# Kernel tuning notes

Measured on AMD Instinct MI355X. Metric: run time of the kernel, lower is better.

The kernel has to match this reference:

```python
import jax, jax.numpy as jnp
import numpy as np

EPS = 1e-5  # F.normalize eps


def _l2norm(x):
    # torch F.normalize(p=2): x / max(||x||, eps)
    n = jnp.sqrt(jnp.sum(x * x, axis=-1, keepdims=True))
    return x / jnp.maximum(n, EPS)


def setup_inputs() -> dict:
    B, L, D, T = 32, 128, 256, 10000
    key = jax.random.key(0)
    ks = jax.random.split(key, 10)
    data = jax.random.normal(ks[0], (B, L, D), jnp.float32)
    # event ids in [1, T]; 0 is the padding id (none here, so packing matches original loop)
    event_type = jax.random.randint(ks[1], (B, L), 1, T + 1, dtype=jnp.int32)
    emb_table = jax.random.normal(ks[2], (T + 1, D), jnp.float32)
    place_correlation = jax.random.uniform(ks[3], (T, T), jnp.float32)
    xav = np.sqrt(2.0 / (T + D))  # xavier_normal_ std for Linear(dim, num_types)
    W5 = jax.random.normal(ks[4], (T, D), jnp.float32) * xav
    W1 = jax.random.normal(ks[5], (T, D), jnp.float32) * xav
    W2 = jax.random.normal(ks[6], (T, D), jnp.float32) * xav
    W3 = jax.random.normal(ks[7], (T, D), jnp.float32) * xav
    W4 = jax.random.normal(ks[8], (T, D), jnp.float32) * xav
    one = jnp.ones((1,), jnp.float32)
    # F.dropout(p=0.5, training=True): precomputed keep-mask already scaled by 1/(1-p)=2
    drop_mask = jax.random.bernoulli(ks[9], 0.5, (B, L, T)).astype(jnp.float32) * 2.0
    return dict(data=data, event_type=event_type, emb_table=emb_table,
                place_correlation=place_correlation, W1=W1, W2=W2, W3=W3, W4=W4,
                W5=W5, a=one, b=one, c=one, d=one, drop_mask=drop_mask)


def reference(data, event_type, emb_table, place_correlation,
              W1, W2, W3, W4, W5, a, b, c, d, drop_mask):
    B = data.shape[0]
    T = W5.shape[0]
    # event_emb(event_type).detach()
    event_enc = jax.lax.stop_gradient(emb_table[event_type])           # [B,L,D]
    inner = jnp.tanh(jnp.einsum('bld,td->blt', event_enc, W5)) * drop_mask  # [B,L,T]
    valid = event_type != 0                                            # pad mask
    idx = jnp.where(valid, event_type - 1, 0)                          # [B,L]
    # per-event gather of correlation rows, fused multiply + reduce over L
    corr = place_correlation[idx] * valid[..., None].astype(place_correlation.dtype)  # [B,L,T]
    item = _l2norm(jnp.sum(inner * corr, axis=1))                      # [B,T]
    # target_: ones, zeroed at observed event indices
    rows = jnp.arange(B)[:, None]
    target = jnp.ones((B, T), jnp.float32).at[rows, idx].min(
        jnp.where(valid, 0.0, 1.0).astype(jnp.float32))
    dm = jnp.mean(data, axis=1)                                        # [B,D]
    p = lambda W: _l2norm(dm @ W.T)
    out = jnp.tanh(p(W1) * a + p(W2) * b + p(W3) * c + p(W4) * d + item)
    return out, target
```

## Files before the change

### kernel.cpp

```cpp
#include <hip/hip_runtime.h>
#include <hip/hip_bf16.h>
#include <stdint.h>

#define T_DIM 10000
#define B_DIM 32
#define L_DIM 128
#define D_DIM 256
#define NT_TILES 79
#define TPAD (NT_TILES*128)

typedef __bf16 bf16x8 __attribute__((ext_vector_type(8)));
typedef float  f32x4  __attribute__((ext_vector_type(4)));
typedef unsigned short us8 __attribute__((ext_vector_type(8)));
typedef unsigned short ushort_t;

__device__ __forceinline__ unsigned short f2bf(float f){
  union { float f; uint32_t u; } v; v.f = f;
  uint32_t u = v.u;
  return (unsigned short)((u + 0x7fffu + ((u >> 16) & 1u)) >> 16);
}

__device__ __forceinline__ void async16(const void* g, void* l){
  __builtin_amdgcn_global_load_lds((const __attribute__((address_space(1))) void*)g,
                                   (__attribute__((address_space(3))) void*)l,
                                   16, 0, 0);
}

__device__ __forceinline__ float fast_tanh(float x){
  x = fminf(8.f, fmaxf(-8.f, x));
  float e = __expf(2.f * x);
  return (e - 1.f) * __builtin_amdgcn_rcpf(e + 1.f);
}

__global__ __launch_bounds__(256) void k_prep(
    const float* __restrict__ emb, const int* __restrict__ et,
    const float* __restrict__ W5, const float* __restrict__ data,
    ushort_t* __restrict__ ebf, ushort_t* __restrict__ w5b,
    ushort_t* __restrict__ dmb, float* __restrict__ tgt){
  int bx = blockIdx.x, tid = threadIdx.x;
  if (bx < 1024){
    int r = bx * 4 + (tid >> 6), d4 = tid & 63;
    int e = et[r];
    float4 v = *((const float4*)(emb + (size_t)e * D_DIM) + d4);
    ushort4 o; o.x = f2bf(v.x); o.y = f2bf(v.y); o.z = f2bf(v.z); o.w = f2bf(v.w);
    *((ushort4*)(ebf + (size_t)r * D_DIM) + d4) = o;
  } else if (bx < 3552){
    int r = (bx - 1024) * 4 + (tid >> 6), d4 = tid & 63;
    ushort4 o = {0,0,0,0};
    if (r < T_DIM){
      float4 v = *((const float4*)(W5 + (size_t)r * D_DIM) + d4);
      o.x = f2bf(v.x); o.y = f2bf(v.y); o.z = f2bf(v.z); o.w = f2bf(v.w);
    }
    *((ushort4*)(w5b + (size_t)r * D_DIM) + d4) = o;
  } else if (bx < 3584){
    int b = bx - 3552, d = tid;
    const float* p = data + (size_t)b * L_DIM * D_DIM + d;
    float s = 0.f;
    #pragma unroll 4
    for (int l = 0; l < L_DIM; l++) s += p[(size_t)l * D_DIM];
    dmb[b * D_DIM + d] = f2bf(s * (1.0f / L_DIM));
  } else {
    int i = (bx - 3584) * 256 + tid;
    if (i < B_DIM * T_DIM) tgt[i] = 1.0f;
  }
}

__global__ __launch_bounds__(256, 4) void k_big(
    const ushort_t* __restrict__ ebf, const ushort_t* __restrict__ w5b,
    const float* __restrict__ corr, const float* __restrict__ drop,
    const int* __restrict__ et, float* __restrict__ item){
  __shared__ __align__(16) ushort_t lA[128 * 64];
  __shared__ __align__(16) ushort_t lB[128 * 64];
  const int b  = blockIdx.y;
  const int t0 = blockIdx.x * 128;
  const int tid = threadIdx.x;
  const int w = tid >> 6, lane = tid & 63, col = lane & 15, quad = lane >> 4;
  const int srow8 = lane >> 3, sslot = lane & 7;

  f32x4 zero4 = {0.f, 0.f, 0.f, 0.f};
  f32x4 acc[2][8];
  #pragma unroll
  for (int m = 0; m < 2; m++)
    #pragma unroll
    for (int n = 0; n < 8; n++) acc[m][n] = zero4;

  for (int c = 0; c < 4; c++){
    if (c) __syncthreads();
    #pragma unroll
    for (int it = 0; it < 4; it++){
      int rb = (it * 4 + w) * 8;
      int row = rb + srow8;
      int gseg = sslot ^ (row & 7);
      async16(ebf + (size_t)(b * L_DIM + row) * D_DIM + c * 64 + gseg * 8,
              lA + rb * 64);
      async16(w5b + (size_t)(t0 + row) * D_DIM + c * 64 + gseg * 8,
              lB + rb * 64);
    }
    __syncthreads();
    #pragma unroll
    for (int kk = 0; kk < 2; kk++){
      bf16x8 af[2];
      #pragma unroll
      for (int m = 0; m < 2; m++){
        int row = w * 32 + m * 16 + col;
        int sg = (kk * 4 + quad) ^ (row & 7);
        af[m] = *(const bf16x8*)(lA + row * 64 + sg * 8);
      }
      #pragma unroll
      for (int n = 0; n < 8; n++){
        int row = n * 16 + col;
        int sg = (kk * 4 + quad) ^ (row & 7);
        bf16x8 bf = *(const bf16x8*)(lB + row * 64 + sg * 8);
        acc[0][n] = __builtin_amdgcn_mfma_f32_16x16x32_bf16(af[0], bf, acc[0][n], 0, 0, 0);
        acc[1][n] = __builtin_amdgcn_mfma_f32_16x16x32_bf16(af[1], bf, acc[1][n], 0, 0, 0);
      }
    }
  }
  __syncthreads();

  int doff[8]; int coff[8]; float vm[8];
  #pragma unroll
  for (int m = 0; m < 2; m++)
    #pragma unroll
    for (int j = 0; j < 4; j++){
      int i = m * 4 + j;
      int l = w * 32 + m * 16 + quad * 4 + j;
      int e = et[b * L_DIM + l];
      doff[i] = (b * L_DIM + l) * T_DIM;
      coff[i] = (e > 0 ? e - 1 : 0) * T_DIM;
      vm[i] = (e > 0) ? 1.f : 0.f;
    }

  float* red = (float*)lA;
  #pragma unroll
  for (int n = 0; n < 8; n++){
    int t = t0 + n * 16 + col;
    bool tv = t < T_DIM;
    float s = 0.f;
    #pragma unroll
    for (int m = 0; m < 2; m++)
      #pragma unroll
      for (int j = 0; j < 4; j++){
        int i = m * 4 + j;
        float th = fast_tanh(acc[m][n][j]);
        float dv = tv ? drop[(size_t)doff[i] + t] : 0.f;
        float cv = tv ? corr[(size_t)coff[i] + t] : 0.f;
        s += th * dv * (cv * vm[i]);
      }
    s += __shfl_xor(s, 16);
    s += __shfl_xor(s, 32);
    if (lane < 16) red[w * 128 + n * 16 + col] = s;
  }
  __syncthreads();
  if (tid < 128){
    int t = t0 + tid;
    if (t < T_DIM)
      item[(size_t)b * T_DIM + t] = red[tid] + red[128 + tid] + red[256 + tid] + red[384 + tid];
  }
}

__global__ __launch_bounds__(256) void k_qgemm(
    const float* __restrict__ W1, const float* __restrict__ W2,
    const float* __restrict__ W3, const float* __restrict__ W4,
    const ushort_t* __restrict__ dmb, float* __restrict__ q){
  __shared__ __align__(16) ushort_t lB[128 * 128];
  const int kw = blockIdx.y;
  const float* W = (kw == 0) ? W1 : (kw == 1) ? W2 : (kw == 2) ? W3 : W4;
  const int t0 = blockIdx.x * 128;
  const int tid = threadIdx.x;
  const int w = tid >> 6, lane = tid & 63, col = lane & 15, quad = lane >> 4;

  f32x4 zero4 = {0.f, 0.f, 0.f, 0.f};
  f32x4 acc[2][2];
  acc[0][0] = zero4; acc[0][1] = zero4; acc[1][0] = zero4; acc[1][1] = zero4;

  for (int c = 0; c < 2; c++){
    if (c) __syncthreads();
    #pragma unroll
    for (int it = 0; it < 8; it++){
      int idx = it * 256 + tid;
      int row = idx >> 4, slot = idx & 15;
      int gseg = slot ^ (row & 7);
      int t = t0 + row;
      float4 u0 = {0,0,0,0}, u1 = {0,0,0,0};
      if (t < T_DIM){
        const float* gp = W + (size_t)t * D_DIM + c * 128 + gseg * 8;
        u0 = *(const float4*)gp;
        u1 = *(const float4*)(gp + 4);
      }
      us8 o;
      o[0] = f2bf(u0.x); o[1] = f2bf(u0.y); o[2] = f2bf(u0.z); o[3] = f2bf(u0.w);
      o[4] = f2bf(u1.x); o[5] = f2bf(u1.y); o[6] = f2bf(u1.z); o[7] = f2bf(u1.w);
      *(us8*)(lB + row * 128 + slot * 8) = o;
    }
    __syncthreads();
    #pragma unroll
    for (int kk = 0; kk < 4; kk++){
      int kabs = c * 128 + kk * 32 + quad * 8;
      bf16x8 af[2];
      #pragma unroll
      for (int m = 0; m < 2; m++)
        af[m] = *(const bf16x8*)(dmb + (size_t)(m * 16 + col) * D_DIM + kabs);
      #pragma unroll
      for (int n2 = 0; n2 < 2; n2++){
        int row = (w * 2 + n2) * 16 + col;
        int sg = (kk * 4 + quad) ^ (row & 7);
        bf16x8 bf = *(const bf16x8*)(lB + row * 128 + sg * 8);
        acc[0][n2] = __builtin_amdgcn_mfma_f32_16x16x32_bf16(af[0], bf, acc[0][n2], 0, 0, 0);
        acc[1][n2] = __builtin_amdgcn_mfma_f32_16x16x32_bf16(af[1], bf, acc[1][n2], 0, 0, 0);
      }
    }
  }
  #pragma unroll
  for (int m = 0; m < 2; m++)
    #pragma unroll
    for (int n2 = 0; n2 < 2; n2++)
      #pragma unroll
      for (int j = 0; j < 4; j++){
        int brow = m * 16 + quad * 4 + j;
        int t = t0 + (w * 2 + n2) * 16 + col;
        if (t < T_DIM)
          q[((size_t)kw * B_DIM + brow) * T_DIM + t] = acc[m][n2][j];
      }
}

__global__ __launch_bounds__(256) void k_norms(const float* __restrict__ q,
    const float* __restrict__ item, float* __restrict__ norms,
    const int* __restrict__ et, float* __restrict__ tgt){
  int which = blockIdx.x, b = blockIdx.y;
  if (which == 5){
    if (threadIdx.x < L_DIM){
      int e = et[b * L_DIM + threadIdx.x];
      if (e > 0) tgt[(size_t)b * T_DIM + (e - 1)] = 0.f;
    }
    return;
  }
  const float* src = (which < 4) ? (q + ((size_t)which * B_DIM + b) * T_DIM)
                                 : (item + (size_t)b * T_DIM);
  float s = 0.f;
  for (int i = threadIdx.x; i < T_DIM; i += 256){ float v = src[i]; s = fmaf(v, v, s); }
  #pragma unroll
  for (int o = 1; o < 64; o <<= 1) s += __shfl_xor(s, o);
  __shared__ float tmp[4];
  if ((threadIdx.x & 63) == 0) tmp[threadIdx.x >> 6] = s;
  __syncthreads();
  if (threadIdx.x == 0) norms[which * B_DIM + b] = sqrtf(tmp[0] + tmp[1] + tmp[2] + tmp[3]);
}

__global__ __launch_bounds__(256) void k_final(
    const float* __restrict__ q, const float* __restrict__ item,
    const float* __restrict__ norms,
    const float* __restrict__ pa, const float* __restrict__ pb,
    const float* __restrict__ pc, const float* __restrict__ pd,
    float* __restrict__ out){
  int b = blockIdx.y;
  int t = blockIdx.x * 256 + threadIdx.x;
  if (t >= T_DIM) return;
  float coef0 = *pa, coef1 = *pb, coef2 = *pc, coef3 = *pd;
  float v = item[(size_t)b * T_DIM + t] / fmaxf(norms[4 * B_DIM + b], 1e-5f);
  v += q[((size_t)0 * B_DIM + b) * T_DIM + t] * coef0 / fmaxf(norms[0 * B_DIM + b], 1e-5f);
  v += q[((size_t)1 * B_DIM + b) * T_DIM + t] * coef1 / fmaxf(norms[1 * B_DIM + b], 1e-5f);
  v += q[((size_t)2 * B_DIM + b) * T_DIM + t] * coef2 / fmaxf(norms[2 * B_DIM + b], 1e-5f);
  v += q[((size_t)3 * B_DIM + b) * T_DIM + t] * coef3 / fmaxf(norms[3 * B_DIM + b], 1e-5f);
  out[(size_t)b * T_DIM + t] = tanhf(v);
}

extern "C" void kernel_launch(void* const* d_in, const int* in_sizes, int n_in,
                              void* d_out, int out_size, void* d_ws, size_t ws_size,
                              hipStream_t stream){
  const float* data = (const float*)d_in[0];
  const int*   et   = (const int*)d_in[1];
  const float* emb  = (const float*)d_in[2];
  const float* corr = (const float*)d_in[3];
  const float* W1   = (const float*)d_in[4];
  const float* W2   = (const float*)d_in[5];
  const float* W3   = (const float*)d_in[6];
  const float* W4   = (const float*)d_in[7];
  const float* W5   = (const float*)d_in[8];
  const float* ca   = (const float*)d_in[9];
  const float* cb   = (const float*)d_in[10];
  const float* cc   = (const float*)d_in[11];
  const float* cd   = (const float*)d_in[12];
  const float* drop = (const float*)d_in[13];

  char* p = (char*)d_ws;
  ushort_t* ebf  = (ushort_t*)p; p += (size_t)B_DIM * L_DIM * D_DIM * 2;
  ushort_t* w5b  = (ushort_t*)p; p += (size_t)TPAD * D_DIM * 2;
  ushort_t* dmb  = (ushort_t*)p; p += (size_t)B_DIM * D_DIM * 2;
  float*    q    = (float*)p;    p += (size_t)4 * B_DIM * T_DIM * 4;
  float*    item = (float*)p;    p += (size_t)B_DIM * T_DIM * 4;
  float*    norms= (float*)p;    p += (size_t)5 * B_DIM * 4;

  float* out = (float*)d_out;
  float* tgt = out + (size_t)B_DIM * T_DIM;

  hipLaunchKernelGGL(k_prep,  dim3(4834),            dim3(256), 0, stream,
                     emb, et, W5, data, ebf, w5b, dmb, tgt);
  hipLaunchKernelGGL(k_big,   dim3(NT_TILES, B_DIM), dim3(256), 0, stream,
                     ebf, w5b, corr, drop, et, item);
  hipLaunchKernelGGL(k_qgemm, dim3(NT_TILES, 4),     dim3(256), 0, stream,
                     W1, W2, W3, W4, dmb, q);
  hipLaunchKernelGGL(k_norms, dim3(6, B_DIM),        dim3(256), 0, stream,
                     q, item, norms, et, tgt);
  hipLaunchKernelGGL(k_final, dim3(40, B_DIM),       dim3(256), 0, stream,
                     q, item, norms, ca, cb, cc, cd, out);
}
```

Baseline: 693.1 us.

## Fuse q-GEMM into main kernel and compute norms via atomic accumulation

Merges the W1-W4 projection GEMM into the main tanh/dropout/correlation kernel as extra block rows of one grid. Squared-norm partial sums are now accumulated with atomics in each GEMM epilogue, which removes the separate norms kernel and its re-read of q and item. The target scatter moves into the final kernel. This cuts two launches and one memory pass, but adds atomic traffic and summation order that is no longer deterministic.

```diff
diff --git a/kernel.cpp b/kernel.cpp
--- a/kernel.cpp
+++ b/kernel.cpp
@@ -36,7 +36,8 @@
     const float* __restrict__ emb, const int* __restrict__ et,
     const float* __restrict__ W5, const float* __restrict__ data,
     ushort_t* __restrict__ ebf, ushort_t* __restrict__ w5b,
-    ushort_t* __restrict__ dmb, float* __restrict__ tgt){
+    ushort_t* __restrict__ dmb, float* __restrict__ tgt,
+    float* __restrict__ norms2){
   int bx = blockIdx.x, tid = threadIdx.x;
   if (bx < 1024){
     int r = bx * 4 + (tid >> 6), d4 = tid & 63;
@@ -59,209 +60,211 @@
     #pragma unroll 4
     for (int l = 0; l < L_DIM; l++) s += p[(size_t)l * D_DIM];
     dmb[b * D_DIM + d] = f2bf(s * (1.0f / L_DIM));
-  } else {
+  } else if (bx < 4834){
     int i = (bx - 3584) * 256 + tid;
     if (i < B_DIM * T_DIM) tgt[i] = 1.0f;
+  } else {
+    if (tid < 160) norms2[tid] = 0.f;
   }
 }
 
-__global__ __launch_bounds__(256, 4) void k_big(
+__global__ __launch_bounds__(256, 4) void k_main(
     const ushort_t* __restrict__ ebf, const ushort_t* __restrict__ w5b,
     const float* __restrict__ corr, const float* __restrict__ drop,
-    const int* __restrict__ et, float* __restrict__ item){
-  __shared__ __align__(16) ushort_t lA[128 * 64];
-  __shared__ __align__(16) ushort_t lB[128 * 64];
-  const int b  = blockIdx.y;
+    const int* __restrict__ et, float* __restrict__ item,
+    const float* __restrict__ W1, const float* __restrict__ W2,
+    const float* __restrict__ W3, const float* __restrict__ W4,
+    const ushort_t* __restrict__ dmb, float* __restrict__ q,
+    float* __restrict__ norms2){
+  __shared__ __align__(16) ushort_t smem[128 * 128];
+  __shared__ float ssq[32];
   const int t0 = blockIdx.x * 128;
   const int tid = threadIdx.x;
   const int w = tid >> 6, lane = tid & 63, col = lane & 15, quad = lane >> 4;
-  const int srow8 = lane >> 3, sslot = lane & 7;
-
-  f32x4 zero4 = {0.f, 0.f, 0.f, 0.f};
-  f32x4 acc[2][8];
-  #pragma unroll
-  for (int m = 0; m < 2; m++)
-    #pragma unroll
-    for (int n = 0; n < 8; n++) acc[m][n] = zero4;
-
-  for (int c = 0; c < 4; c++){
-    if (c) __syncthreads();
-    #pragma unroll
-    for (int it = 0; it < 4; it++){
-      int rb = (it * 4 + w) * 8;
-      int row = rb + srow8;
-      int gseg = sslot ^ (row & 7);
-      async16(ebf + (size_t)(b * L_DIM + row) * D_DIM + c * 64 + gseg * 8,
-              lA + rb * 64);
-      async16(w5b + (size_t)(t0 + row) * D_DIM + c * 64 + gseg * 8,
-              lB + rb * 64);
+
+  if (blockIdx.y < B_DIM){
+    ushort_t* lA = smem;
+    ushort_t* lB = smem + 128 * 64;
+    const int b = blockIdx.y;
+    const int srow8 = lane >> 3, sslot = lane & 7;
+
+    f32x4 zero4 = {0.f, 0.f, 0.f, 0.f};
+    f32x4 acc[2][8];
+    #pragma unroll
+    for (int m = 0; m < 2; m++)
+      #pragma unroll
+      for (int n = 0; n < 8; n++) acc[m][n] = zero4;
+
+    for (int c = 0; c < 4; c++){
+      if (c) __syncthreads();
+      #pragma unroll
+      for (int it = 0; it < 4; it++){
+        int rb = (it * 4 + w) * 8;
+        int row = rb + srow8;
+        int gseg = sslot ^ (row & 7);
+        async16(ebf + (size_t)(b * L_DIM + row) * D_DIM + c * 64 + gseg * 8,
+                lA + rb * 64);
+        async16(w5b + (size_t)(t0 + row) * D_DIM + c * 64 + gseg * 8,
+                lB + rb * 64);
+      }
+      __syncthreads();
+      #pragma unroll
+      for (int kk = 0; kk < 2; kk++){
+        bf16x8 af[2];
+        #pragma unroll
+        for (int m = 0; m < 2; m++){
+          int row = w * 32 + m * 16 + col;
+          int sg = (kk * 4 + quad) ^ (row & 7);
+          af[m] = *(const bf16x8*)(lA + row * 64 + sg * 8);
+        }
+        #pragma unroll
+        for (int n = 0; n < 8; n++){
+          int row = n * 16 + col;
+          int sg = (kk * 4 + quad) ^ (row & 7);
+          bf16x8 bf = *(const bf16x8*)(lB + row * 64 + sg * 8);
+          acc[0][n] = __builtin_amdgcn_mfma_f32_16x16x32_bf16(af[0], bf, acc[0][n], 0, 0, 0);
+          acc[1][n] = __builtin_amdgcn_mfma_f32_16x16x32_bf16(af[1], bf, acc[1][n], 0, 0, 0);
+        }
+      }
     }
     __syncthreads();
-    #pragma unroll
-    for (int kk = 0; kk < 2; kk++){
-      bf16x8 af[2];
-      #pragma unroll
-      for (int m = 0; m < 2; m++){
-        int row = w * 32 + m * 16 + col;
-        int sg = (kk * 4 + quad) ^ (row & 7);
-        af[m] = *(const bf16x8*)(lA + row * 64 + sg * 8);
-      }
-      #pragma unroll
-      for (int n = 0; n < 8; n++){
-        int row = n * 16 + col;
-        int sg = (kk * 4 + quad) ^ (row & 7);
-        bf16x8 bf = *(const bf16x8*)(lB + row * 64 + sg * 8);
-        acc[0][n] = __builtin_amdgcn_mfma_f32_16x16x32_bf16(af[0], bf, acc[0][n], 0, 0, 0);
-        acc[1][n] = __builtin_amdgcn_mfma_f32_16x16x32_bf16(af[1], bf, acc[1][n], 0, 0, 0);
-      }
-    }
-  }
-  __syncthreads();
-
-  int doff[8]; int coff[8]; float vm[8];
-  #pragma unroll
-  for (int m = 0; m < 2; m++)
-    #pragma unroll
-    for (int j = 0; j < 4; j++){
-      int i = m * 4 + j;
-      int l = w * 32 + m * 16 + quad * 4 + j;
-      int e = et[b * L_DIM + l];
-      doff[i] = (b * L_DIM + l) * T_DIM;
-      coff[i] = (e > 0 ? e - 1 : 0) * T_DIM;
-      vm[i] = (e > 0) ? 1.f : 0.f;
-    }
-
-  float* red = (float*)lA;
-  #pragma unroll
-  for (int n = 0; n < 8; n++){
-    int t = t0 + n * 16 + col;
-    bool tv = t < T_DIM;
-    float s = 0.f;
+
+    int doff[8]; int coff[8]; float vm[8];
     #pragma unroll
     for (int m = 0; m < 2; m++)
       #pragma unroll
       for (int j = 0; j < 4; j++){
         int i = m * 4 + j;
-        float th = fast_tanh(acc[m][n][j]);
-        float dv = tv ? drop[(size_t)doff[i] + t] : 0.f;
-        float cv = tv ? corr[(size_t)coff[i] + t] : 0.f;
-        s += th * dv * (cv * vm[i]);
-      }
-    s += __shfl_xor(s, 16);
-    s += __shfl_xor(s, 32);
-    if (lane < 16) red[w * 128 + n * 16 + col] = s;
+        int l = w * 32 + m * 16 + quad * 4 + j;
+        int e = et[b * L_DIM + l];
+        doff[i] = (b * L_DIM + l) * T_DIM;
+        coff[i] = (e > 0 ? e - 1 : 0) * T_DIM;
+        vm[i] = (e > 0) ? 1.f : 0.f;
+      }
+
+    float* red = (float*)smem;
+    #pragma unroll
+    for (int n = 0; n < 8; n++){
+      int t = t0 + n * 16 + col;
+      bool tv = t < T_DIM;
+      float s = 0.f;
+      #pragma unroll
+      for (int m = 0; m < 2; m++)
+        #pragma unroll
+        for (int j = 0; j < 4; j++){
+          int i = m * 4 + j;
+          float th = fast_tanh(acc[m][n][j]);
+          float dv = tv ? drop[(size_t)doff[i] + t] : 0.f;
+          float cv = tv ? corr[(size_t)coff[i] + t] : 0.f;
+          s += th * dv * (cv * vm[i]);
+        }
+      s += __shfl_xor(s, 16);
+      s += __shfl_xor(s, 32);
+      if (lane < 16) red[w * 128 + n * 16 + col] = s;
+    }
+    __syncthreads();
+    float sv = 0.f;
+    if (tid < 128){
+      int t = t0 + tid;
+      if (t < T_DIM){
+        float v = red[tid] + red[128 + tid] + red[256 + tid] + red[384 + tid];
+        item[(size_t)b * T_DIM + t] = v;
+        sv = v * v;
+      }
+    }
+    #pragma unroll
+    for (int o = 1; o < 64; o <<= 1) sv += __shfl_xor(sv, o);
+    if (lane == 0 && sv != 0.f) atomicAdd(&norms2[128 + b], sv);
+  } else {
+    ushort_t* lB = smem;
+    const int kw = blockIdx.y - B_DIM;
+    const float* W = (kw == 0) ? W1 : (kw == 1) ? W2 : (kw == 2) ? W3 : W4;
+
+    f32x4 zero4 = {0.f, 0.f, 0.f, 0.f};
+    f32x4 acc[2][2];
+    acc[0][0] = zero4; acc[0][1] = zero4; acc[1][0] = zero4; acc[1][1] = zero4;
+    if (tid < 32) ssq[tid] = 0.f;
+
+    for (int c = 0; c < 2; c++){
+      if (c) __syncthreads();
+      #pragma unroll
+      for (int it = 0; it < 8; it++){
+        int idx = it * 256 + tid;
+        int row = idx >> 4, slot = idx & 15;
+        int gseg = slot ^ (row & 7);
+        int t = t0 + row;
+        float4 u0 = {0,0,0,0}, u1 = {0,0,0,0};
+        if (t < T_DIM){
+          const float* gp = W + (size_t)t * D_DIM + c * 128 + gseg * 8;
+          u0 = *(const float4*)gp;
+          u1 = *(const float4*)(gp + 4);
+        }
+        us8 o;
+        o[0] = f2bf(u0.x); o[1] = f2bf(u0.y); o[2] = f2bf(u0.z); o[3] = f2bf(u0.w);
+        o[4] = f2bf(u1.x); o[5] = f2bf(u1.y); o[6] = f2bf(u1.z); o[7] = f2bf(u1.w);
+        *(us8*)(lB + row * 128 + slot * 8) = o;
+      }
+      __syncthreads();
+      #pragma unroll
+      for (int kk = 0; kk < 4; kk++){
+        int kabs = c * 128 + kk * 32 + quad * 8;
+        bf16x8 af[2];
+        #pragma unroll
+        for (int m = 0; m < 2; m++)
+          af[m] = *(const bf16x8*)(dmb + (size_t)(m * 16 + col) * D_DIM + kabs);
+        #pragma unroll
+        for (int n2 = 0; n2 < 2; n2++){
+          int row = (w * 2 + n2) * 16 + col;
+          int sg = (kk * 4 + quad) ^ (row & 7);
+          bf16x8 bf = *(const bf16x8*)(lB + row * 128 + sg * 8);
+          acc[0][n2] = __builtin_amdgcn_mfma_f32_16x16x32_bf16(af[0], bf, acc[0][n2], 0, 0, 0);
+          acc[1][n2] = __builtin_amdgcn_mfma_f32_16x16x32_bf16(af[1], bf, acc[1][n2], 0, 0, 0);
+        }
+      }
+    }
+    __syncthreads();
+    #pragma unroll
+    for (int m = 0; m < 2; m++)
+      #pragma unroll
+      for (int n2 = 0; n2 < 2; n2++)
+        #pragma unroll
+        for (int j = 0; j < 4; j++){
+          int brow = m * 16 + quad * 4 + j;
+          int t = t0 + (w * 2 + n2) * 16 + col;
+          if (t < T_DIM){
+            float v = acc[m][n2][j];
+            q[((size_t)kw * B_DIM + brow) * T_DIM + t] = v;
+            atomicAdd(&ssq[brow], v * v);
+          }
+        }
+    __syncthreads();
+    if (tid < 32) atomicAdd(&norms2[kw * 32 + tid], ssq[tid]);
   }
-  __syncthreads();
-  if (tid < 128){
-    int t = t0 + tid;
-    if (t < T_DIM)
-      item[(size_t)b * T_DIM + t] = red[tid] + red[128 + tid] + red[256 + tid] + red[384 + tid];
-  }
-}
-
-__global__ __launch_bounds__(256) void k_qgemm(
-    const float* __restrict__ W1, const float* __restrict__ W2,
-    const float* __restrict__ W3, const float* __restrict__ W4,
-    const ushort_t* __restrict__ dmb, float* __restrict__ q){
-  __shared__ __align__(16) ushort_t lB[128 * 128];
-  const int kw = blockIdx.y;
-  const float* W = (kw == 0) ? W1 : (kw == 1) ? W2 : (kw == 2) ? W3 : W4;
-  const int t0 = blockIdx.x * 128;
-  const int tid = threadIdx.x;
-  const int w = tid >> 6, lane = tid & 63, col = lane & 15, quad = lane >> 4;
-
-  f32x4 zero4 = {0.f, 0.f, 0.f, 0.f};
-  f32x4 acc[2][2];
-  acc[0][0] = zero4; acc[0][1] = zero4; acc[1][0] = zero4; acc[1][1] = zero4;
-
-  for (int c = 0; c < 2; c++){
-    if (c) __syncthreads();
-    #pragma unroll
-    for (int it = 0; it < 8; it++){
-      int idx = it * 256 + tid;
-      int row = idx >> 4, slot = idx & 15;
-      int gseg = slot ^ (row & 7);
-      int t = t0 + row;
-      float4 u0 = {0,0,0,0}, u1 = {0,0,0,0};
-      if (t < T_DIM){
-        const float* gp = W + (size_t)t * D_DIM + c * 128 + gseg * 8;
-        u0 = *(const float4*)gp;
-        u1 = *(const float4*)(gp + 4);
-      }
-      us8 o;
-      o[0] = f2bf(u0.x); o[1] = f2bf(u0.y); o[2] = f2bf(u0.z); o[3] = f2bf(u0.w);
-      o[4] = f2bf(u1.x); o[5] = f2bf(u1.y); o[6] = f2bf(u1.z); o[7] = f2bf(u1.w);
-      *(us8*)(lB + row * 128 + slot * 8) = o;
-    }
-    __syncthreads();
-    #pragma unroll
-    for (int kk = 0; kk < 4; kk++){
-      int kabs = c * 128 + kk * 32 + quad * 8;
-      bf16x8 af[2];
-      #pragma unroll
-      for (int m = 0; m < 2; m++)
-        af[m] = *(const bf16x8*)(dmb + (size_t)(m * 16 + col) * D_DIM + kabs);
-      #pragma unroll
-      for (int n2 = 0; n2 < 2; n2++){
-        int row = (w * 2 + n2) * 16 + col;
-        int sg = (kk * 4 + quad) ^ (row & 7);
-        bf16x8 bf = *(const bf16x8*)(lB + row * 128 + sg * 8);
-        acc[0][n2] = __builtin_amdgcn_mfma_f32_16x16x32_bf16(af[0], bf, acc[0][n2], 0, 0, 0);
-        acc[1][n2] = __builtin_amdgcn_mfma_f32_16x16x32_bf16(af[1], bf, acc[1][n2], 0, 0, 0);
-      }
-    }
-  }
-  #pragma unroll
-  for (int m = 0; m < 2; m++)
-    #pragma unroll
-    for (int n2 = 0; n2 < 2; n2++)
-      #pragma unroll
-      for (int j = 0; j < 4; j++){
-        int brow = m * 16 + quad * 4 + j;
-        int t = t0 + (w * 2 + n2) * 16 + col;
-        if (t < T_DIM)
-          q[((size_t)kw * B_DIM + brow) * T_DIM + t] = acc[m][n2][j];
-      }
-}
-
-__global__ __launch_bounds__(256) void k_norms(const float* __restrict__ q,
-    const float* __restrict__ item, float* __restrict__ norms,
-    const int* __restrict__ et, float* __restrict__ tgt){
-  int which = blockIdx.x, b = blockIdx.y;
-  if (which == 5){
+}
+
+__global__ __launch_bounds__(256) void k_final(
+    const float* __restrict__ q, const float* __restrict__ item,
+    const float* __restrict__ norms2,
+    const float* __restrict__ pa, const float* __restrict__ pb,
+    const float* __restrict__ pc, const float* __restrict__ pd,
+    float* __restrict__ out, float* __restrict__ tgt,
+    const int* __restrict__ et){
+  int b = blockIdx.y;
+  if (blockIdx.x == 40){
     if (threadIdx.x < L_DIM){
       int e = et[b * L_DIM + threadIdx.x];
       if (e > 0) tgt[(size_t)b * T_DIM + (e - 1)] = 0.f;
     }
     return;
   }
-  const float* src = (which < 4) ? (q + ((size_t)which * B_DIM + b) * T_DIM)
-                                 : (item + (size_t)b * T_DIM);
-  float s = 0.f;
-  for (int i = threadIdx.x; i < T_DIM; i += 256){ float v = src[i]; s = fmaf(v, v, s); }
-  #pragma unroll
-  for (int o = 1; o < 64; o <<= 1) s += __shfl_xor(s, o);
-  __shared__ float tmp[4];
-  if ((threadIdx.x & 63) == 0) tmp[threadIdx.x >> 6] = s;
-  __syncthreads();
-  if (threadIdx.x == 0) norms[which * B_DIM + b] = sqrtf(tmp[0] + tmp[1] + tmp[2] + tmp[3]);
-}
-
-__global__ __launch_bounds__(256) void k_final(
-    const float* __restrict__ q, const float* __restrict__ item,
-    const float* __restrict__ norms,
-    const float* __restrict__ pa, const float* __restrict__ pb,
-    const float* __restrict__ pc, const float* __restrict__ pd,
-    float* __restrict__ out){
-  int b = blockIdx.y;
   int t = blockIdx.x * 256 + threadIdx.x;
   if (t >= T_DIM) return;
-  float coef0 = *pa, coef1 = *pb, coef2 = *pc, coef3 = *pd;
-  float v = item[(size_t)b * T_DIM + t] / fmaxf(norms[4 * B_DIM + b], 1e-5f);
-  v += q[((size_t)0 * B_DIM + b) * T_DIM + t] * coef0 / fmaxf(norms[0 * B_DIM + b], 1e-5f);
-  v += q[((size_t)1 * B_DIM + b) * T_DIM + t] * coef1 / fmaxf(norms[1 * B_DIM + b], 1e-5f);
-  v += q[((size_t)2 * B_DIM + b) * T_DIM + t] * coef2 / fmaxf(norms[2 * B_DIM + b], 1e-5f);
-  v += q[((size_t)3 * B_DIM + b) * T_DIM + t] * coef3 / fmaxf(norms[3 * B_DIM + b], 1e-5f);
+  float coef[4] = {*pa, *pb, *pc, *pd};
+  float v = item[(size_t)b * T_DIM + t] / fmaxf(sqrtf(norms2[128 + b]), 1e-5f);
+  #pragma unroll
+  for (int k = 0; k < 4; k++)
+    v += q[((size_t)k * B_DIM + b) * T_DIM + t] * coef[k]
+         / fmaxf(sqrtf(norms2[k * 32 + b]), 1e-5f);
   out[(size_t)b * T_DIM + t] = tanhf(v);
 }
 
@@ -289,19 +292,15 @@
   ushort_t* dmb  = (ushort_t*)p; p += (size_t)B_DIM * D_DIM * 2;
   float*    q    = (float*)p;    p += (size_t)4 * B_DIM * T_DIM * 4;
   float*    item = (float*)p;    p += (size_t)B_DIM * T_DIM * 4;
-  float*    norms= (float*)p;    p += (size_t)5 * B_DIM * 4;
+  float*    norms2=(float*)p;    p += (size_t)160 * 4;
 
   float* out = (float*)d_out;
   float* tgt = out + (size_t)B_DIM * T_DIM;
 
-  hipLaunchKernelGGL(k_prep,  dim3(4834),            dim3(256), 0, stream,
-                     emb, et, W5, data, ebf, w5b, dmb, tgt);
-  hipLaunchKernelGGL(k_big,   dim3(NT_TILES, B_DIM), dim3(256), 0, stream,
-                     ebf, w5b, corr, drop, et, item);
-  hipLaunchKernelGGL(k_qgemm, dim3(NT_TILES, 4),     dim3(256), 0, stream,
-                     W1, W2, W3, W4, dmb, q);
-  hipLaunchKernelGGL(k_norms, dim3(6, B_DIM),        dim3(256), 0, stream,
-                     q, item, norms, et, tgt);
-  hipLaunchKernelGGL(k_final, dim3(40, B_DIM),       dim3(256), 0, stream,
-                     q, item, norms, ca, cb, cc, cd, out);
-}
+  hipLaunchKernelGGL(k_prep,  dim3(4835),                dim3(256), 0, stream,
+                     emb, et, W5, data, ebf, w5b, dmb, tgt, norms2);
+  hipLaunchKernelGGL(k_main,  dim3(NT_TILES, B_DIM + 4), dim3(256), 0, stream,
+                     ebf, w5b, corr, drop, et, item, W1, W2, W3, W4, dmb, q, norms2);
+  hipLaunchKernelGGL(k_final, dim3(41, B_DIM),           dim3(256), 0, stream,
+                     q, item, norms2, ca, cb, cc, cd, out, tgt, et);
+}
```

After: 688.2 us. About the same (-0.7%).
